# Kernel tuning notes

Hardware: AMD Instinct MI355X
Metric: run time of the kernel (lower is better)

The kernel has to match this reference:

```python
import jax, jax.numpy as jnp
import numpy as np

N_HEAD = 16
N_EMBD = 1024
TIME_EMBD = 64
EPS = 1e-5

def _ln(x, w, b):
    mu = jnp.mean(x, axis=-1, keepdims=True)
    var = jnp.mean(jnp.square(x - mu), axis=-1, keepdims=True)
    return (x - mu) * jax.lax.rsqrt(var + EPS) * w + b

def _gelu(x):
    return jax.nn.gelu(x, approximate=False)

def setup_inputs() -> dict:
    key = jax.random.key(0)
    ks = jax.random.split(key, 12)
    B, T, D, TE = 2, 2048, N_EMBD, TIME_EMBD
    C = D + TE  # 1088
    s = lambda fan_in: 1.0 / np.sqrt(fan_in)
    return {
        "z": jax.random.normal(ks[0], (B, T, D), jnp.float32),
        "t": jax.random.uniform(ks[1], (B,), jnp.float32),
        # time_mlp: Linear(1, TE) -> GELU -> Linear(TE, TE)
        "w_t1": jax.random.normal(ks[2], (1, TE), jnp.float32) * s(1),
        "b_t1": jnp.zeros((TE,), jnp.float32),
        "w_t2": jax.random.normal(ks[3], (TE, TE), jnp.float32) * s(TE),
        "b_t2": jnp.zeros((TE,), jnp.float32),
        # attention
        "ln_a_w": jnp.ones((C,), jnp.float32),
        "ln_a_b": jnp.zeros((C,), jnp.float32),
        "w_attn": jax.random.normal(ks[4], (C, 3 * D), jnp.float32) * s(C),
        "b_attn": jnp.zeros((3 * D,), jnp.float32),
        "w_proj": jax.random.normal(ks[5], (D, D), jnp.float32) * s(D),
        "b_proj": jnp.zeros((D,), jnp.float32),
        # mlp
        "ln_m_w": jnp.ones((C,), jnp.float32),
        "ln_m_b": jnp.zeros((C,), jnp.float32),
        "w_fc": jax.random.normal(ks[6], (C, 4 * D), jnp.float32) * s(C),
        "b_fc": jnp.zeros((4 * D,), jnp.float32),
        "w_fc2": jax.random.normal(ks[7], (4 * D, D), jnp.float32) * s(4 * D),
        "b_fc2": jnp.zeros((D,), jnp.float32),
    }

def reference(z, t, w_t1, b_t1, w_t2, b_t2, ln_a_w, ln_a_b, w_attn, b_attn,
              w_proj, b_proj, ln_m_w, ln_m_b, w_fc, b_fc, w_fc2, b_fc2):
    B, T, D = z.shape
    H, hd = N_HEAD, N_EMBD // N_HEAD
    # time embedding: [B, TE] broadcast over T
    t_emb = _gelu(t[:, None] @ w_t1 + b_t1) @ w_t2 + b_t2
    t_emb_bt = jnp.broadcast_to(t_emb[:, None, :], (B, T, TIME_EMBD))
    # --- attention with time-conditioned input ---
    zt = jnp.concatenate([z, t_emb_bt], axis=-1)            # [B,T,D+TE]
    x = _ln(zt, ln_a_w, ln_a_b)
    qkv = x @ w_attn + b_attn                               # [B,T,3D]
    q, k, v = jnp.split(qkv, 3, axis=-1)
    q = q.reshape(B, T, H, hd)
    k = k.reshape(B, T, H, hd)
    v = v.reshape(B, T, H, hd)
    att = jnp.einsum('bqhd,bkhd->bhqk', q, k) * (1.0 / np.sqrt(hd))
    mask = jnp.tril(jnp.ones((T, T), bool))
    att = jnp.where(mask, att, -jnp.inf)
    att = jax.nn.softmax(att, axis=-1)
    y = jnp.einsum('bhqk,bkhd->bqhd', att, v).reshape(B, T, D)
    h = y @ w_proj + b_proj                                 # [B,T,D]
    # --- mlp with time-conditioned input ---
    ht = jnp.concatenate([h, t_emb_bt], axis=-1)
    m = _ln(ht, ln_m_w, ln_m_b)
    dz = _gelu(m @ w_fc + b_fc) @ w_fc2 + b_fc2             # [B,T,D]
    return dz
```

## Files before the change

kernel.cpp:

```cpp
#include <hip/hip_runtime.h>
#include <stdint.h>
#include <math.h>

#define T_SEQ 2048
#define NHEAD 16
#define HD 64
#define DMODEL 1024
#define CDIM 1088
#define MROWS 4096

typedef uint16_t u16;
typedef __bf16 b8v __attribute__((ext_vector_type(8)));
typedef float f4v __attribute__((ext_vector_type(4)));

typedef __attribute__((address_space(3))) void lds_void;
typedef const __attribute__((address_space(1))) void glb_void;

__device__ __forceinline__ float b2f(u16 u) {
  union { uint32_t i; float f; } c; c.i = ((uint32_t)u) << 16; return c.f;
}
__device__ __forceinline__ u16 f2b(float f) {
  union { float f; uint32_t i; } c; c.f = f;
  uint32_t x = c.i;
  return (u16)((x + 0x7fffu + ((x >> 16) & 1u)) >> 16);
}
__device__ __forceinline__ float gelu_f(float x) {
  return 0.5f * x * (1.0f + erff(x * 0.70710678118654752f));
}

__global__ void time_mlp_kernel(const float* __restrict__ t, const float* __restrict__ w1,
                                const float* __restrict__ b1, const float* __restrict__ w2,
                                const float* __restrict__ b2, float* __restrict__ temb) {
  __shared__ float h1[2][64];
  int tid = threadIdx.x;
  int b = tid >> 6, i = tid & 63;
  float tv = t[b];
  h1[b][i] = gelu_f(tv * w1[i] + b1[i]);
  __syncthreads();
  float acc = b2[i];
  for (int k = 0; k < 64; ++k) acc += h1[b][k] * w2[k * 64 + i];
  temb[b * 64 + i] = acc;
}

__global__ __launch_bounds__(256) void transpose_kernel(const float* __restrict__ src,
                                                        u16* __restrict__ dst,
                                                        int R, int C) {
  __shared__ u16 tile[32][33];
  int tx = threadIdx.x & 31, ty = threadIdx.x >> 5;
  int c0 = blockIdx.x * 32, r0 = blockIdx.y * 32;
#pragma unroll
  for (int i = 0; i < 4; ++i) {
    int r = ty + i * 8;
    tile[r][tx] = f2b(src[(size_t)(r0 + r) * C + c0 + tx]);
  }
  __syncthreads();
#pragma unroll
  for (int i = 0; i < 4; ++i) {
    int c = ty + i * 8;
    dst[(size_t)(c0 + c) * R + r0 + tx] = tile[tx][c];
  }
}

__global__ __launch_bounds__(256) void add2_kernel(const float4* __restrict__ a,
                                                   const float4* __restrict__ b,
                                                   float4* __restrict__ o, int n4) {
  int i = blockIdx.x * 256 + threadIdx.x;
  if (i < n4) {
    float4 x = a[i], y = b[i];
    o[i] = float4{x.x + y.x, x.y + y.y, x.z + y.z, x.w + y.w};
  }
}

__global__ __launch_bounds__(256) void ln_concat_kernel(const float* __restrict__ zf,
                                                        const float* __restrict__ zf2,
                                                        const u16* __restrict__ zb,
                                                        const float* __restrict__ temb,
                                                        const float* __restrict__ w,
                                                        const float* __restrict__ bvec,
                                                        u16* __restrict__ xout,
                                                        int mode) {
  __shared__ float red[4];
  int row = blockIdx.x;
  int b = row / T_SEQ;
  int tid = threadIdx.x;
  float v[5];
  float sum = 0.f;
#pragma unroll
  for (int i = 0; i < 5; ++i) {
    int c = tid + i * 256;
    float val = 0.f;
    if (c < CDIM) {
      if (c < DMODEL) {
        size_t idx = (size_t)row * DMODEL + c;
        if (mode == 0) val = b2f(zb[idx]);
        else if (mode == 1) val = zf[idx];
        else val = zf[idx] + zf2[idx];
      } else {
        val = temb[b * 64 + (c - DMODEL)];
      }
    }
    v[i] = val;
    sum += val;
  }
#pragma unroll
  for (int off = 32; off; off >>= 1) sum += __shfl_xor(sum, off, 64);
  int wv = tid >> 6, ln = tid & 63;
  if (ln == 0) red[wv] = sum;
  __syncthreads();
  float mean = (red[0] + red[1] + red[2] + red[3]) * (1.0f / CDIM);
  __syncthreads();
  float sq = 0.f;
#pragma unroll
  for (int i = 0; i < 5; ++i) {
    int c = tid + i * 256;
    if (c < CDIM) { float d = v[i] - mean; sq += d * d; }
  }
#pragma unroll
  for (int off = 32; off; off >>= 1) sq += __shfl_xor(sq, off, 64);
  if (ln == 0) red[wv] = sq;
  __syncthreads();
  float inv = rsqrtf((red[0] + red[1] + red[2] + red[3]) * (1.0f / CDIM) + 1e-5f);
#pragma unroll
  for (int i = 0; i < 5; ++i) {
    int c = tid + i * 256;
    if (c < CDIM)
      xout[(size_t)row * CDIM + c] = f2b((v[i] - mean) * inv * w[c] + bvec[c]);
  }
}

__global__ __launch_bounds__(256) void gemm_bt_kernel(const u16* __restrict__ A,
                                                      const u16* __restrict__ Bt,
                                                      const float* __restrict__ bias,
                                                      void* __restrict__ Cout,
                                                      int M, int N, int K,
                                                      int do_gelu, int out_f32) {
  __shared__ u16 As[2][128 * 32];
  __shared__ u16 Bs[2][128 * 32];
  const int tid = threadIdx.x;
  const int wave = tid >> 6, lane = tid & 63;
  const int wr = wave >> 1, wc = wave & 1;
  const int m0 = blockIdx.x * 128;
  const int n0 = blockIdx.y * 128;
  const int lrow = lane & 15, quad = lane >> 4;
  const int srow = lane >> 2, sseg = lane & 3;

  const u16* gA0 = A  + (size_t)(m0 + wave * 32 + srow) * K + sseg * 8;
  const u16* gA1 = gA0 + (size_t)16 * K;
  const u16* gB0 = Bt + (size_t)(n0 + wave * 32 + srow) * K + sseg * 8;
  const u16* gB1 = gB0 + (size_t)16 * K;
  const int la0 = (wave * 32) * 32, la1 = (wave * 32 + 16) * 32;

  f4v acc[4][4] = {};

  __builtin_amdgcn_global_load_lds((glb_void*)gA0, (lds_void*)&As[0][la0], 16, 0, 0);
  __builtin_amdgcn_global_load_lds((glb_void*)gA1, (lds_void*)&As[0][la1], 16, 0, 0);
  __builtin_amdgcn_global_load_lds((glb_void*)gB0, (lds_void*)&Bs[0][la0], 16, 0, 0);
  __builtin_amdgcn_global_load_lds((glb_void*)gB1, (lds_void*)&Bs[0][la1], 16, 0, 0);

  int cur = 0;
  for (int k0 = 0; k0 < K; k0 += 32) {
    __syncthreads();
    if (k0 + 32 < K) {
      int nxt = cur ^ 1;
      __builtin_amdgcn_global_load_lds((glb_void*)(gA0 + k0 + 32), (lds_void*)&As[nxt][la0], 16, 0, 0);
      __builtin_amdgcn_global_load_lds((glb_void*)(gA1 + k0 + 32), (lds_void*)&As[nxt][la1], 16, 0, 0);
      __builtin_amdgcn_global_load_lds((glb_void*)(gB0 + k0 + 32), (lds_void*)&Bs[nxt][la0], 16, 0, 0);
      __builtin_amdgcn_global_load_lds((glb_void*)(gB1 + k0 + 32), (lds_void*)&Bs[nxt][la1], 16, 0, 0);
    }
    b8v af[4], bfr[4];
#pragma unroll
    for (int mi = 0; mi < 4; ++mi)
      af[mi] = *(const b8v*)(&As[cur][(wr * 64 + mi * 16 + lrow) * 32 + quad * 8]);
#pragma unroll
    for (int ni = 0; ni < 4; ++ni)
      bfr[ni] = *(const b8v*)(&Bs[cur][(wc * 64 + ni * 16 + lrow) * 32 + quad * 8]);
#pragma unroll
    for (int mi = 0; mi < 4; ++mi)
#pragma unroll
      for (int ni = 0; ni < 4; ++ni)
        acc[mi][ni] = __builtin_amdgcn_mfma_f32_16x16x32_bf16(af[mi], bfr[ni], acc[mi][ni], 0, 0, 0);
    cur ^= 1;
  }

#pragma unroll
  for (int mi = 0; mi < 4; ++mi) {
#pragma unroll
    for (int ni = 0; ni < 4; ++ni) {
      int gcol = n0 + wc * 64 + ni * 16 + lrow;
      float bv = bias[gcol];
#pragma unroll
      for (int r = 0; r < 4; ++r) {
        int grow = m0 + wr * 64 + mi * 16 + quad * 4 + r;
        float v = acc[mi][ni][r] + bv;
        if (do_gelu) v = gelu_f(v);
        if (out_f32)
          ((float*)Cout)[(size_t)grow * N + gcol] = v;
        else
          ((u16*)Cout)[(size_t)grow * N + gcol] = f2b(v);
      }
    }
  }
}

__global__ __launch_bounds__(256) void gemm_splitk2_kernel(const u16* __restrict__ A,
                                                           const u16* __restrict__ Bt,
                                                           const float* __restrict__ bias,
                                                           float* __restrict__ C0,
                                                           float* __restrict__ C1,
                                                           int M, int N, int K, int Kc) {
  __shared__ u16 As[2][128 * 32];
  __shared__ u16 Bs[2][128 * 32];
  const int tid = threadIdx.x;
  const int wave = tid >> 6, lane = tid & 63;
  const int wr = wave >> 1, wc = wave & 1;
  const int m0 = blockIdx.x * 128;
  const int n0 = blockIdx.y * 128;
  const int kz = blockIdx.z;
  const int lrow = lane & 15, quad = lane >> 4;
  const int srow = lane >> 2, sseg = lane & 3;

  const u16* gA0 = A  + (size_t)(m0 + wave * 32 + srow) * K + kz * Kc + sseg * 8;
  const u16* gA1 = gA0 + (size_t)16 * K;
  const u16* gB0 = Bt + (size_t)(n0 + wave * 32 + srow) * K + kz * Kc + sseg * 8;
  const u16* gB1 = gB0 + (size_t)16 * K;
  const int la0 = (wave * 32) * 32, la1 = (wave * 32 + 16) * 32;

  f4v acc[4][4] = {};

  __builtin_amdgcn_global_load_lds((glb_void*)gA0, (lds_void*)&As[0][la0], 16, 0, 0);
  __builtin_amdgcn_global_load_lds((glb_void*)gA1, (lds_void*)&As[0][la1], 16, 0, 0);
  __builtin_amdgcn_global_load_lds((glb_void*)gB0, (lds_void*)&Bs[0][la0], 16, 0, 0);
  __builtin_amdgcn_global_load_lds((glb_void*)gB1, (lds_void*)&Bs[0][la1], 16, 0, 0);

  int cur = 0;
  for (int k0 = 0; k0 < Kc; k0 += 32) {
    __syncthreads();
    if (k0 + 32 < Kc) {
      int nxt = cur ^ 1;
      __builtin_amdgcn_global_load_lds((glb_void*)(gA0 + k0 + 32), (lds_void*)&As[nxt][la0], 16, 0, 0);
      __builtin_amdgcn_global_load_lds((glb_void*)(gA1 + k0 + 32), (lds_void*)&As[nxt][la1], 16, 0, 0);
      __builtin_amdgcn_global_load_lds((glb_void*)(gB0 + k0 + 32), (lds_void*)&Bs[nxt][la0], 16, 0, 0);
      __builtin_amdgcn_global_load_lds((glb_void*)(gB1 + k0 + 32), (lds_void*)&Bs[nxt][la1], 16, 0, 0);
    }
    b8v af[4], bfr[4];
#pragma unroll
    for (int mi = 0; mi < 4; ++mi)
      af[mi] = *(const b8v*)(&As[cur][(wr * 64 + mi * 16 + lrow) * 32 + quad * 8]);
#pragma unroll
    for (int ni = 0; ni < 4; ++ni)
      bfr[ni] = *(const b8v*)(&Bs[cur][(wc * 64 + ni * 16 + lrow) * 32 + quad * 8]);
#pragma unroll
    for (int mi = 0; mi < 4; ++mi)
#pragma unroll
      for (int ni = 0; ni < 4; ++ni)
        acc[mi][ni] = __builtin_amdgcn_mfma_f32_16x16x32_bf16(af[mi], bfr[ni], acc[mi][ni], 0, 0, 0);
    cur ^= 1;
  }

  float* C = kz ? C1 : C0;
#pragma unroll
  for (int mi = 0; mi < 4; ++mi) {
#pragma unroll
    for (int ni = 0; ni < 4; ++ni) {
      int gcol = n0 + wc * 64 + ni * 16 + lrow;
      float bv = (kz == 0) ? bias[gcol] : 0.f;
#pragma unroll
      for (int r = 0; r < 4; ++r) {
        int grow = m0 + wr * 64 + mi * 16 + quad * 4 + r;
        C[(size_t)grow * N + gcol] = acc[mi][ni][r] + bv;
      }
    }
  }
}

__global__ __launch_bounds__(256) void attn_mfma_kernel(const u16* __restrict__ qkv,
                                                        u16* __restrict__ y) {
  __shared__ u16 Ks[64 * 72];
  __shared__ u16 Vts[64 * 72];
  __shared__ u16 Ps[64 * 72];
  const int bh = blockIdx.x;
  const int b = bh >> 4, h = bh & 15;
  const int qt = 31 - blockIdx.y;
  const int tid = threadIdx.x, w = tid >> 6, lane = tid & 63;
  const int lrow = lane & 15, quad = lane >> 4;
  const int q0 = qt * 64;
  const int qg = q0 + w * 16 + lrow;

  b8v qf[2];
#pragma unroll
  for (int dc = 0; dc < 2; ++dc)
    qf[dc] = *(const b8v*)(qkv + (size_t)(b * T_SEQ + qg) * 3072 + h * 64 + dc * 32 + quad * 8);

  f4v oacc[4] = {};
  float mrun = -__builtin_inff(), lrun = 0.f;

  const int nch = qt + 1;
  for (int ct = 0; ct < nch; ++ct) {
    __syncthreads();
    {
      int r = tid >> 2, sg = tid & 3;
      const u16* src = qkv + (size_t)(b * T_SEQ + ct * 64 + r) * 3072 + h * 64 + 1024 + sg * 16;
      *(uint4*)(&Ks[r * 72 + sg * 16]) = *(const uint4*)(src);
      *(uint4*)(&Ks[r * 72 + sg * 16 + 8]) = *(const uint4*)(src + 8);
    }
    {
      int pr = tid >> 3, dsg = tid & 7;
      const u16* v0 = qkv + (size_t)(b * T_SEQ + ct * 64 + 2 * pr) * 3072 + h * 64 + 2048 + dsg * 8;
      uint4 a = *(const uint4*)(v0);
      uint4 bb = *(const uint4*)(v0 + 3072);
      uint32_t aw[4] = {a.x, a.y, a.z, a.w};
      uint32_t bw[4] = {bb.x, bb.y, bb.z, bb.w};
#pragma unroll
      for (int j = 0; j < 8; ++j) {
        int d = dsg * 8 + j;
        u16 ae = (u16)(aw[j >> 1] >> ((j & 1) * 16));
        u16 be = (u16)(bw[j >> 1] >> ((j & 1) * 16));
        int keyp = (2 * pr) ^ (((d >> 3) & 7) * 8);
        *(uint32_t*)(&Vts[d * 72 + keyp]) = (uint32_t)ae | ((uint32_t)be << 16);
      }
    }
    __syncthreads();

    f4v sacc[4] = {};
#pragma unroll
    for (int ks = 0; ks < 4; ++ks)
#pragma unroll
      for (int dc = 0; dc < 2; ++dc) {
        b8v kf = *(const b8v*)(&Ks[(ks * 16 + lrow) * 72 + dc * 32 + quad * 8]);
        sacc[ks] = __builtin_amdgcn_mfma_f32_16x16x32_bf16(kf, qf[dc], sacc[ks], 0, 0, 0);
      }

    bool diag = (ct == qt);
#pragma unroll
    for (int ks = 0; ks < 4; ++ks)
#pragma unroll
      for (int r = 0; r < 4; ++r) {
        float v = sacc[ks][r] * 0.125f;
        int key = ct * 64 + ks * 16 + quad * 4 + r;
        if (diag && key > qg) v = -__builtin_inff();
        sacc[ks][r] = v;
      }

    float rmax = sacc[0][0];
#pragma unroll
    for (int ks = 0; ks < 4; ++ks)
#pragma unroll
      for (int r = 0; r < 4; ++r) rmax = fmaxf(rmax, sacc[ks][r]);
    rmax = fmaxf(rmax, __shfl_xor(rmax, 16, 64));
    rmax = fmaxf(rmax, __shfl_xor(rmax, 32, 64));
    float mn = fmaxf(mrun, rmax);
    float al = __expf(mrun - mn);
    mrun = mn;
    float psum = 0.f;
#pragma unroll
    for (int ks = 0; ks < 4; ++ks)
#pragma unroll
      for (int r = 0; r < 4; ++r) {
        float p = __expf(sacc[ks][r] - mn);
        sacc[ks][r] = p;
        psum += p;
      }
    psum += __shfl_xor(psum, 16, 64);
    psum += __shfl_xor(psum, 32, 64);
    lrun = lrun * al + psum;
#pragma unroll
    for (int ds = 0; ds < 4; ++ds) oacc[ds] *= al;

#pragma unroll
    for (int ks = 0; ks < 4; ++ks) {
      ushort4 pw;
      pw.x = f2b(sacc[ks][0]); pw.y = f2b(sacc[ks][1]);
      pw.z = f2b(sacc[ks][2]); pw.w = f2b(sacc[ks][3]);
      *(ushort4*)(&Ps[(w * 16 + lrow) * 72 + ks * 16 + quad * 4]) = pw;
    }

    b8v pf[2];
#pragma unroll
    for (int kc = 0; kc < 2; ++kc)
      pf[kc] = *(const b8v*)(&Ps[(w * 16 + lrow) * 72 + kc * 32 + quad * 8]);
#pragma unroll
    for (int ds = 0; ds < 4; ++ds)
#pragma unroll
      for (int kc = 0; kc < 2; ++kc) {
        int d = ds * 16 + lrow;
        int off = (kc * 32 + quad * 8) ^ (((d >> 3) & 7) * 8);
        b8v vfv = *(const b8v*)(&Vts[d * 72 + off]);
        oacc[ds] = __builtin_amdgcn_mfma_f32_16x16x32_bf16(vfv, pf[kc], oacc[ds], 0, 0, 0);
      }
  }

  float rinv = 1.0f / lrun;
  u16* yrow = y + (size_t)(b * T_SEQ + qg) * DMODEL + h * 64;
#pragma unroll
  for (int ds = 0; ds < 4; ++ds) {
    ushort4 ov;
    ov.x = f2b(oacc[ds][0] * rinv);
    ov.y = f2b(oacc[ds][1] * rinv);
    ov.z = f2b(oacc[ds][2] * rinv);
    ov.w = f2b(oacc[ds][3] * rinv);
    *(ushort4*)(yrow + ds * 16 + quad * 4) = ov;
  }
}

extern "C" void kernel_launch(void* const* d_in, const int* in_sizes, int n_in,
                              void* d_out, int out_size, void* d_ws, size_t ws_size,
                              hipStream_t stream) {
  const float* z      = (const float*)d_in[0];
  const float* t      = (const float*)d_in[1];
  const float* w_t1   = (const float*)d_in[2];
  const float* b_t1   = (const float*)d_in[3];
  const float* w_t2   = (const float*)d_in[4];
  const float* b_t2   = (const float*)d_in[5];
  const float* ln_a_w = (const float*)d_in[6];
  const float* ln_a_b = (const float*)d_in[7];
  const float* w_attn = (const float*)d_in[8];
  const float* b_attn = (const float*)d_in[9];
  const float* w_proj = (const float*)d_in[10];
  const float* b_proj = (const float*)d_in[11];
  const float* ln_m_w = (const float*)d_in[12];
  const float* ln_m_b = (const float*)d_in[13];
  const float* w_fc   = (const float*)d_in[14];
  const float* b_fc   = (const float*)d_in[15];
  const float* w_fc2  = (const float*)d_in[16];
  const float* b_fc2  = (const float*)d_in[17];

  char* ws = (char*)d_ws;
  float* temb  = (float*)ws;
  u16* wT_attn = (u16*)(ws + 1024);
  u16* wT_proj = wT_attn + (size_t)3072 * 1088;
  u16* wT_fc   = wT_proj + (size_t)1024 * 1024;
  u16* wT_fc2  = wT_fc   + (size_t)4096 * 1088;
  u16* xbuf    = wT_fc2  + (size_t)1024 * 4096;
  u16* big     = xbuf    + (size_t)4096 * 1088;
  u16* ybuf    = big     + (size_t)4096 * 4096;
  float* p0    = (float*)(ybuf + (size_t)4096 * 1024);
  float* p1    = p0 + (size_t)4096 * 1024;

  time_mlp_kernel<<<dim3(1), dim3(128), 0, stream>>>(t, w_t1, b_t1, w_t2, b_t2, temb);

  transpose_kernel<<<dim3(3072 / 32, 1088 / 32), dim3(256), 0, stream>>>(w_attn, wT_attn, 1088, 3072);
  transpose_kernel<<<dim3(1024 / 32, 1024 / 32), dim3(256), 0, stream>>>(w_proj, wT_proj, 1024, 1024);
  transpose_kernel<<<dim3(4096 / 32, 1088 / 32), dim3(256), 0, stream>>>(w_fc, wT_fc, 1088, 4096);
  transpose_kernel<<<dim3(1024 / 32, 4096 / 32), dim3(256), 0, stream>>>(w_fc2, wT_fc2, 4096, 1024);

  ln_concat_kernel<<<dim3(MROWS), dim3(256), 0, stream>>>(
      z, (const float*)nullptr, (const u16*)nullptr, temb, ln_a_w, ln_a_b, xbuf, 1);

  gemm_bt_kernel<<<dim3(MROWS / 128, 3072 / 128), dim3(256), 0, stream>>>(
      xbuf, wT_attn, b_attn, big, MROWS, 3072, 1088, 0, 0);

  attn_mfma_kernel<<<dim3(32, 32), dim3(256), 0, stream>>>(big, ybuf);

  gemm_splitk2_kernel<<<dim3(MROWS / 128, 1024 / 128, 2), dim3(256), 0, stream>>>(
      ybuf, wT_proj, b_proj, p0, p1, MROWS, 1024, 1024, 512);

  ln_concat_kernel<<<dim3(MROWS), dim3(256), 0, stream>>>(
      p0, p1, (const u16*)nullptr, temb, ln_m_w, ln_m_b, xbuf, 2);

  gemm_bt_kernel<<<dim3(MROWS / 128, 4096 / 128), dim3(256), 0, stream>>>(
      xbuf, wT_fc, b_fc, big, MROWS, 4096, 1088, 1, 0);

  gemm_splitk2_kernel<<<dim3(MROWS / 128, 1024 / 128, 2), dim3(256), 0, stream>>>(
      big, wT_fc2, b_fc2, p0, p1, MROWS, 1024, 4096, 2048);

  add2_kernel<<<dim3((MROWS * 1024 / 4 + 255) / 256), dim3(256), 0, stream>>>(
      (const float4*)p0, (const float4*)p1, (float4*)d_out, MROWS * 1024 / 4);
}
```

Measured before the change: 407.0 us.

## Give each wave private LDS tiles and replace block barriers with vmcnt waits

Both GEMM kernels now have every wave load its own 64-row A and B slices into a per-wave double-buffered LDS region. This removes the per-iteration __syncthreads, with each wave waiting on its own outstanding global-to-LDS loads through s_waitcnt vmcnt. The aim is to drop block-wide barrier stalls so waves run independently. In exchange, each A and B row slice is now loaded twice, once by each wave that shares it, which doubles global and L2 traffic. LDS use also doubles to 64KB, which may lower occupancy.

```diff
diff --git a/kernel.cpp b/kernel.cpp
--- a/kernel.cpp
+++ b/kernel.cpp
@@ -15,6 +15,9 @@
 
 typedef __attribute__((address_space(3))) void lds_void;
 typedef const __attribute__((address_space(1))) void glb_void;
+
+#define WAITCNT_VM8 0xF78
+#define WAITCNT_VM0 0xF70
 
 __device__ __forceinline__ float b2f(u16 u) {
   union { uint32_t i; float f; } c; c.i = ((uint32_t)u) << 16; return c.f;
@@ -134,46 +137,51 @@
                                                       void* __restrict__ Cout,
                                                       int M, int N, int K,
                                                       int do_gelu, int out_f32) {
-  __shared__ u16 As[2][128 * 32];
-  __shared__ u16 Bs[2][128 * 32];
+  __shared__ u16 Aw[4][2][64 * 32];
+  __shared__ u16 Bw[4][2][64 * 32];
   const int tid = threadIdx.x;
   const int wave = tid >> 6, lane = tid & 63;
   const int wr = wave >> 1, wc = wave & 1;
   const int m0 = blockIdx.x * 128;
   const int n0 = blockIdx.y * 128;
   const int lrow = lane & 15, quad = lane >> 4;
-  const int srow = lane >> 2, sseg = lane & 3;
-
-  const u16* gA0 = A  + (size_t)(m0 + wave * 32 + srow) * K + sseg * 8;
-  const u16* gA1 = gA0 + (size_t)16 * K;
-  const u16* gB0 = Bt + (size_t)(n0 + wave * 32 + srow) * K + sseg * 8;
-  const u16* gB1 = gB0 + (size_t)16 * K;
-  const int la0 = (wave * 32) * 32, la1 = (wave * 32 + 16) * 32;
+  const int srow = lane >> 2;
+
+  const u16* gA = A  + (size_t)(m0 + wr * 64 + srow) * K + (lane & 3) * 8;
+  const u16* gB = Bt + (size_t)(n0 + wc * 64 + srow) * K + (lane & 3) * 8;
 
   f4v acc[4][4] = {};
 
-  __builtin_amdgcn_global_load_lds((glb_void*)gA0, (lds_void*)&As[0][la0], 16, 0, 0);
-  __builtin_amdgcn_global_load_lds((glb_void*)gA1, (lds_void*)&As[0][la1], 16, 0, 0);
-  __builtin_amdgcn_global_load_lds((glb_void*)gB0, (lds_void*)&Bs[0][la0], 16, 0, 0);
-  __builtin_amdgcn_global_load_lds((glb_void*)gB1, (lds_void*)&Bs[0][la1], 16, 0, 0);
+#pragma unroll
+  for (int i = 0; i < 4; ++i) {
+    __builtin_amdgcn_global_load_lds((glb_void*)(gA + (size_t)(i * 16) * K),
+                                     (lds_void*)&Aw[wave][0][i * 16 * 32], 16, 0, 0);
+    __builtin_amdgcn_global_load_lds((glb_void*)(gB + (size_t)(i * 16) * K),
+                                     (lds_void*)&Bw[wave][0][i * 16 * 32], 16, 0, 0);
+  }
 
   int cur = 0;
   for (int k0 = 0; k0 < K; k0 += 32) {
-    __syncthreads();
     if (k0 + 32 < K) {
       int nxt = cur ^ 1;
-      __builtin_amdgcn_global_load_lds((glb_void*)(gA0 + k0 + 32), (lds_void*)&As[nxt][la0], 16, 0, 0);
-      __builtin_amdgcn_global_load_lds((glb_void*)(gA1 + k0 + 32), (lds_void*)&As[nxt][la1], 16, 0, 0);
-      __builtin_amdgcn_global_load_lds((glb_void*)(gB0 + k0 + 32), (lds_void*)&Bs[nxt][la0], 16, 0, 0);
-      __builtin_amdgcn_global_load_lds((glb_void*)(gB1 + k0 + 32), (lds_void*)&Bs[nxt][la1], 16, 0, 0);
+#pragma unroll
+      for (int i = 0; i < 4; ++i) {
+        __builtin_amdgcn_global_load_lds((glb_void*)(gA + (size_t)(i * 16) * K + k0 + 32),
+                                         (lds_void*)&Aw[wave][nxt][i * 16 * 32], 16, 0, 0);
+        __builtin_amdgcn_global_load_lds((glb_void*)(gB + (size_t)(i * 16) * K + k0 + 32),
+                                         (lds_void*)&Bw[wave][nxt][i * 16 * 32], 16, 0, 0);
+      }
+      __builtin_amdgcn_s_waitcnt(WAITCNT_VM8);
+    } else {
+      __builtin_amdgcn_s_waitcnt(WAITCNT_VM0);
     }
     b8v af[4], bfr[4];
 #pragma unroll
     for (int mi = 0; mi < 4; ++mi)
-      af[mi] = *(const b8v*)(&As[cur][(wr * 64 + mi * 16 + lrow) * 32 + quad * 8]);
+      af[mi] = *(const b8v*)(&Aw[wave][cur][(mi * 16 + lrow) * 32 + quad * 8]);
 #pragma unroll
     for (int ni = 0; ni < 4; ++ni)
-      bfr[ni] = *(const b8v*)(&Bs[cur][(wc * 64 + ni * 16 + lrow) * 32 + quad * 8]);
+      bfr[ni] = *(const b8v*)(&Bw[wave][cur][(ni * 16 + lrow) * 32 + quad * 8]);
 #pragma unroll
     for (int mi = 0; mi < 4; ++mi)
 #pragma unroll
@@ -208,8 +216,8 @@
                                                            float* __restrict__ C0,
                                                            float* __restrict__ C1,
                                                            int M, int N, int K, int Kc) {
-  __shared__ u16 As[2][128 * 32];
-  __shared__ u16 Bs[2][128 * 32];
+  __shared__ u16 Aw[4][2][64 * 32];
+  __shared__ u16 Bw[4][2][64 * 32];
   const int tid = threadIdx.x;
   const int wave = tid >> 6, lane = tid & 63;
   const int wr = wave >> 1, wc = wave & 1;
@@ -217,38 +225,43 @@
   const int n0 = blockIdx.y * 128;
   const int kz = blockIdx.z;
   const int lrow = lane & 15, quad = lane >> 4;
-  const int srow = lane >> 2, sseg = lane & 3;
-
-  const u16* gA0 = A  + (size_t)(m0 + wave * 32 + srow) * K + kz * Kc + sseg * 8;
-  const u16* gA1 = gA0 + (size_t)16 * K;
-  const u16* gB0 = Bt + (size_t)(n0 + wave * 32 + srow) * K + kz * Kc + sseg * 8;
-  const u16* gB1 = gB0 + (size_t)16 * K;
-  const int la0 = (wave * 32) * 32, la1 = (wave * 32 + 16) * 32;
+  const int srow = lane >> 2;
+
+  const u16* gA = A  + (size_t)(m0 + wr * 64 + srow) * K + kz * Kc + (lane & 3) * 8;
+  const u16* gB = Bt + (size_t)(n0 + wc * 64 + srow) * K + kz * Kc + (lane & 3) * 8;
 
   f4v acc[4][4] = {};
 
-  __builtin_amdgcn_global_load_lds((glb_void*)gA0, (lds_void*)&As[0][la0], 16, 0, 0);
-  __builtin_amdgcn_global_load_lds((glb_void*)gA1, (lds_void*)&As[0][la1], 16, 0, 0);
-  __builtin_amdgcn_global_load_lds((glb_void*)gB0, (lds_void*)&Bs[0][la0], 16, 0, 0);
-  __builtin_amdgcn_global_load_lds((glb_void*)gB1, (lds_void*)&Bs[0][la1], 16, 0, 0);
+#pragma unroll
+  for (int i = 0; i < 4; ++i) {
+    __builtin_amdgcn_global_load_lds((glb_void*)(gA + (size_t)(i * 16) * K),
+                                     (lds_void*)&Aw[wave][0][i * 16 * 32], 16, 0, 0);
+    __builtin_amdgcn_global_load_lds((glb_void*)(gB + (size_t)(i * 16) * K),
+                                     (lds_void*)&Bw[wave][0][i * 16 * 32], 16, 0, 0);
+  }
 
   int cur = 0;
   for (int k0 = 0; k0 < Kc; k0 += 32) {
-    __syncthreads();
     if (k0 + 32 < Kc) {
       int nxt = cur ^ 1;
-      __builtin_amdgcn_global_load_lds((glb_void*)(gA0 + k0 + 32), (lds_void*)&As[nxt][la0], 16, 0, 0);
-      __builtin_amdgcn_global_load_lds((glb_void*)(gA1 + k0 + 32), (lds_void*)&As[nxt][la1], 16, 0, 0);
-      __builtin_amdgcn_global_load_lds((glb_void*)(gB0 + k0 + 32), (lds_void*)&Bs[nxt][la0], 16, 0, 0);
-      __builtin_amdgcn_global_load_lds((glb_void*)(gB1 + k0 + 32), (lds_void*)&Bs[nxt][la1], 16, 0, 0);
+#pragma unroll
+      for (int i = 0; i < 4; ++i) {
+        __builtin_amdgcn_global_load_lds((glb_void*)(gA + (size_t)(i * 16) * K + k0 + 32),
+                                         (lds_void*)&Aw[wave][nxt][i * 16 * 32], 16, 0, 0);
+        __builtin_amdgcn_global_load_lds((glb_void*)(gB + (size_t)(i * 16) * K + k0 + 32),
+                                         (lds_void*)&Bw[wave][nxt][i * 16 * 32], 16, 0, 0);
+      }
+      __builtin_amdgcn_s_waitcnt(WAITCNT_VM8);
+    } else {
+      __builtin_amdgcn_s_waitcnt(WAITCNT_VM0);
     }
     b8v af[4], bfr[4];
 #pragma unroll
     for (int mi = 0; mi < 4; ++mi)
-      af[mi] = *(const b8v*)(&As[cur][(wr * 64 + mi * 16 + lrow) * 32 + quad * 8]);
+      af[mi] = *(const b8v*)(&Aw[wave][cur][(mi * 16 + lrow) * 32 + quad * 8]);
 #pragma unroll
     for (int ni = 0; ni < 4; ++ni)
-      bfr[ni] = *(const b8v*)(&Bs[cur][(wc * 64 + ni * 16 + lrow) * 32 + quad * 8]);
+      bfr[ni] = *(const b8v*)(&Bw[wave][cur][(ni * 16 + lrow) * 32 + quad * 8]);
 #pragma unroll
     for (int mi = 0; mi < 4; ++mi)
 #pragma unroll
```

After: 440.6 us. 8.3% more time.
